# Performance work log

Hardware: AMD Instinct MI355X
Metric: run time of the kernel (lower is better)

The kernel has to match this reference:

```python
import jax, jax.numpy as jnp
import numpy as np


def _mha(q, k, v, num_heads):
    # q,k,v: [B, L, C] -> multi-head attention, scale = 1/sqrt(head_dim)
    B, Lq, C = q.shape
    Lk = k.shape[1]
    d = C // num_heads
    qh = q.reshape(B, Lq, num_heads, d)
    kh = k.reshape(B, Lk, num_heads, d)
    vh = v.reshape(B, Lk, num_heads, d)
    scale = 1.0 / jnp.sqrt(jnp.asarray(d, q.dtype))
    scores = jnp.einsum('blhd,bmhd->bhlm', qh, kh) * scale
    probs = jax.nn.softmax(scores, axis=-1)
    out = jnp.einsum('bhlm,bmhd->blhd', probs, vh)
    return out.reshape(B, Lq, C)


def setup_inputs() -> dict:
    key = jax.random.key(0)
    ks = jax.random.split(key, 9)
    b, n, f, l, C = 1, 4, 8, 256, 320
    s = 0.02
    return {
        'hidden_states': jax.random.normal(ks[0], (b * n * f, l, C), jnp.float32),
        'Wq': jax.random.normal(ks[1], (C, C), jnp.float32) * s,
        'Wk': jax.random.normal(ks[2], (C, C), jnp.float32) * s,
        'Wv': jax.random.normal(ks[3], (C, C), jnp.float32) * s,
        'Wo': jax.random.normal(ks[4], (C, C), jnp.float32) * s,
        'bo': jnp.zeros((C,), jnp.float32),
        'Wq_i2v': jax.random.normal(ks[5], (C, C), jnp.float32) * s,
        'Wo_i2v': jax.random.normal(ks[6], (C, C), jnp.float32) * s,
        'bo_i2v': jnp.zeros((C,), jnp.float32),
        'num_heads': 8,
        'num_views': 4,
        'num_frames': 8,
    }


def reference(hidden_states, Wq, Wk, Wv, Wo, bo, Wq_i2v, Wo_i2v, bo_i2v,
              num_heads, num_views, num_frames):
    BNF, l, C = hidden_states.shape
    n, f = num_views, num_frames
    b = BNF // (n * f)
    # '(b n f) l c -> (b f) (n l) c'
    h = hidden_states.reshape(b, n, f, l, C).transpose(0, 2, 1, 3, 4).reshape(b * f, n * l, C)
    L = n * l

    q = h @ Wq
    k = h @ Wk
    v = h @ Wv

    # first-frame KV broadcast across all frames within the same b
    k_first = jnp.broadcast_to(k.reshape(b, f, L, C)[:, 0:1], (b, f, L, C)).reshape(b * f, L, C)
    v_first = jnp.broadcast_to(v.reshape(b, f, L, C)[:, 0:1], (b, f, L, C)).reshape(b * f, L, C)

    base = _mha(q, k, v, num_heads)

    q_i2v = h @ Wq_i2v
    i2v = _mha(q_i2v, k_first, v_first, num_heads)
    i2v = i2v @ Wo_i2v + bo_i2v

    out = (base + i2v) @ Wo + bo

    # '(b f) (n l) c -> (b n f) l c'
    out = out.reshape(b, f, n, l, C).transpose(0, 2, 1, 3, 4).reshape(b * n * f, l, C)
    return out
```

## Files before the change

kernel.cpp:

```cpp
#include <hip/hip_runtime.h>

#define MROWS 8192
#define CDIM  320
#define QPAD  512

typedef __attribute__((ext_vector_type(8))) short bf16x8;
typedef __attribute__((ext_vector_type(4))) float f32x4;

__device__ __forceinline__ unsigned bfbits(float x) {
  union { float f; unsigned u; } a; a.f = x;
  return a.u + 0x8000u;
}
__device__ __forceinline__ unsigned pack2bf(float a, float b) {
  return (bfbits(a) >> 16) | (bfbits(b) & 0xffff0000u);
}
__device__ __forceinline__ void splitbf(float x, short& hi, short& lo) {
  unsigned hu = bfbits(x) & 0xffff0000u;
  union { unsigned u; float f; } h; h.u = hu;
  hi = (short)(hu >> 16);
  lo = (short)(bfbits(x - h.f) >> 16);
}

__device__ __forceinline__ int swizzle_row(int r) {
  int ff = r >> 10;
  int t  = r & 1023;
  int nn = t >> 8;
  int ll = t & 255;
  return nn * 2048 + ff * 256 + ll;
}

__global__ __launch_bounds__(256) void wc_kernel(
    const float* __restrict__ Woi, const float* __restrict__ Wo,
    float* __restrict__ Wc)
{
  const int r0 = blockIdx.x * 64, c0 = blockIdx.y * 64;
  __shared__ float As[64][36];
  __shared__ float Bs[32][68];
  const int tid = threadIdx.x, tx = tid & 15, ty = tid >> 4;
  float acc[4][4] = {};

  const int ra = tid >> 3, kq = (tid & 7) * 4;
  const int kb = tid >> 4, cq = (tid & 15) * 4;

  for (int k0 = 0; k0 < 320; k0 += 32) {
    float4 a1 = *(const float4*)(Woi + (size_t)(r0 + ra) * 320 + k0 + kq);
    float4 a2 = *(const float4*)(Woi + (size_t)(r0 + ra + 32) * 320 + k0 + kq);
    float4 b1 = *(const float4*)(Wo + (size_t)(k0 + kb) * 320 + c0 + cq);
    float4 b2 = *(const float4*)(Wo + (size_t)(k0 + kb + 16) * 320 + c0 + cq);
    __syncthreads();
    *(float4*)&As[ra][kq] = a1;
    *(float4*)&As[ra + 32][kq] = a2;
    *(float4*)&Bs[kb][cq] = b1;
    *(float4*)&Bs[kb + 16][cq] = b2;
    __syncthreads();
    #pragma unroll
    for (int kk = 0; kk < 32; ++kk) {
      float4 bv = *(const float4*)&Bs[kk][tx * 4];
      #pragma unroll
      for (int i = 0; i < 4; ++i) {
        float a = As[ty * 4 + i][kk];
        acc[i][0] = fmaf(a, bv.x, acc[i][0]);
        acc[i][1] = fmaf(a, bv.y, acc[i][1]);
        acc[i][2] = fmaf(a, bv.z, acc[i][2]);
        acc[i][3] = fmaf(a, bv.w, acc[i][3]);
      }
    }
  }
  #pragma unroll
  for (int i = 0; i < 4; ++i) {
    float4 v = make_float4(acc[i][0], acc[i][1], acc[i][2], acc[i][3]);
    *(float4*)(Wc + (size_t)(r0 + ty * 4 + i) * 320 + c0 + tx * 4) = v;
  }
}

__global__ __launch_bounds__(256) void pack_kernel(
    const float* __restrict__ hidden,
    const float* __restrict__ Wq, const float* __restrict__ Wk,
    const float* __restrict__ Wv, const float* __restrict__ Wqi,
    const float* __restrict__ Wo, const float* __restrict__ Wc,
    const float* __restrict__ bo, const float* __restrict__ boi,
    short* __restrict__ Ah, short* __restrict__ Al,
    short* __restrict__ WTh, short* __restrict__ WTl,
    short* __restrict__ WFh, short* __restrict__ WFl,
    float* __restrict__ bc,
    short* __restrict__ Qp, short* __restrict__ Kp, short* __restrict__ Qip,
    float qscale)
{
  const int b = blockIdx.x, tid = threadIdx.x;
  if (b < 64) {
    const int r0 = b * 128;
    for (int e = tid; e < 128 * 80; e += 256) {
      int r = e / 80, cq = (e % 80) * 4;
      float4 x = *(const float4*)(hidden + (size_t)swizzle_row(r0 + r) * 320 + cq);
      union { ushort4 v; short s[4]; } h, l;
      splitbf(x.x, h.s[0], l.s[0]); splitbf(x.y, h.s[1], l.s[1]);
      splitbf(x.z, h.s[2], l.s[2]); splitbf(x.w, h.s[3], l.s[3]);
      *(ushort4*)&Ah[(size_t)(r0 + r) * 320 + cq] = h.v;
      *(ushort4*)&Al[(size_t)(r0 + r) * 320 + cq] = l.v;
    }
  } else if (b < 128) {
    const int t2 = b - 64, wi = t2 >> 4, seg = t2 & 15;
    const float* W = wi == 0 ? Wq : wi == 1 ? Wk : wi == 2 ? Wv : Wqi;
    const float s = (wi == 0 || wi == 3) ? qscale : 1.0f;
    short* th = WTh + (size_t)wi * 320 * 320;
    short* tl = WTl + (size_t)wi * 320 * 320;
    for (int e = tid; e < 20 * 320; e += 256) {
      int n = seg * 20 + e / 320, k = e % 320;
      short hi, lo;
      splitbf(W[(size_t)k * 320 + n] * s, hi, lo);
      th[(size_t)n * 320 + k] = hi;
      tl[(size_t)n * 320 + k] = lo;
    }
  } else if (b < 160) {
    const int t2 = b - 128;
    for (int e = tid; e < 10 * 640; e += 256) {
      int n = t2 * 10 + e / 640, k = e % 640;
      float x = (k < 320) ? Wo[(size_t)k * 320 + n] : Wc[(size_t)(k - 320) * 320 + n];
      short hi, lo;
      splitbf(x, hi, lo);
      WFh[(size_t)n * 640 + k] = hi;
      WFl[(size_t)n * 640 + k] = lo;
    }
  } else if (b < 168) {
    const int n = (b - 160) * 40 + tid;
    if (tid < 40) {
      float s = bo[n];
      for (int j = 0; j < 320; ++j) s = fmaf(boi[j], Wo[(size_t)j * 320 + n], s);
      bc[n] = s;
    }
  } else {
    const int bz = b - 168, buf = bz >> 5, seg = bz & 31;
    short* P = buf == 0 ? Qp : buf == 1 ? Kp : Qip;
    const uint4 z = make_uint4(0, 0, 0, 0);
    for (int e = tid; e < 256 * 24; e += 256) {
      int row = (seg << 8) + (e / 24);
      int cc = e % 24, h = cc / 3, c3 = cc % 3;
      *(uint4*)&P[(size_t)row * QPAD + h * 64 + 40 + c3 * 8] = z;
    }
  }
}

__global__ __launch_bounds__(256, 3) void mfma_gemm(
    const short* __restrict__ Ah, const short* __restrict__ Al,
    const short* __restrict__ BTh, const short* __restrict__ BTl,
    int K, int mode,
    short* __restrict__ Qp, short* __restrict__ Kp,
    short* __restrict__ Vt, short* __restrict__ Qip,
    float* __restrict__ Of, const float* __restrict__ bias)
{
  const int tid  = threadIdx.x;
  const int wave = tid >> 6;
  const int lane = tid & 63;
  const int quad = lane >> 4;
  const int l16  = lane & 15;
  const int row0 = blockIdx.x * 128;

  const short *bth, *btl;
  int nbase, wi = 0;
  if (mode == 0) {
    const int ct = blockIdx.y;
    wi = ct / 5;
    bth = BTh + (size_t)wi * 320 * 320;
    btl = BTl + (size_t)wi * 320 * 320;
    nbase = (ct % 5) * 64;
  } else {
    bth = BTh; btl = BTl;
    nbase = blockIdx.y * 64;
  }

  __shared__ short Ash[128][40], Asl[128][40];
  __shared__ short Bsh[64][40],  Bsl[64][40];

  f32x4 acc[2][4];
  #pragma unroll
  for (int mt = 0; mt < 2; ++mt)
    #pragma unroll
    for (int nt = 0; nt < 4; ++nt) acc[mt][nt] = (f32x4){0.f, 0.f, 0.f, 0.f};

  const int ar = tid >> 2, akc = (tid & 3) * 8;
  const int bn = tid >> 2, bkc = (tid & 3) * 8;

  const short* pa_h = Ah + (size_t)(row0 + ar) * K + akc;
  const short* pa_l = Al ? Al + (size_t)(row0 + ar) * K + akc : nullptr;
  const short* pb_h = bth + (size_t)(nbase + bn) * K + bkc;
  const short* pb_l = btl + (size_t)(nbase + bn) * K + bkc;

  for (int k0 = 0; k0 < K; k0 += 32) {
    uint4 ah1 = *(const uint4*)(pa_h + k0);
    uint4 ah2 = *(const uint4*)(pa_h + (size_t)64 * K + k0);
    uint4 al1, al2;
    if (Al) {
      al1 = *(const uint4*)(pa_l + k0);
      al2 = *(const uint4*)(pa_l + (size_t)64 * K + k0);
    }
    uint4 bh = *(const uint4*)(pb_h + k0);
    uint4 bl = *(const uint4*)(pb_l + k0);
    __syncthreads();
    *(uint4*)&Ash[ar][akc]      = ah1;
    *(uint4*)&Ash[ar + 64][akc] = ah2;
    if (Al) {
      *(uint4*)&Asl[ar][akc]      = al1;
      *(uint4*)&Asl[ar + 64][akc] = al2;
    }
    *(uint4*)&Bsh[bn][bkc] = bh;
    *(uint4*)&Bsl[bn][bkc] = bl;
    __syncthreads();

    bf16x8 afh[2], afl[2], bfh[4], bfl[4];
    #pragma unroll
    for (int mt = 0; mt < 2; ++mt) {
      afh[mt] = *(const bf16x8*)&Ash[wave * 32 + mt * 16 + l16][quad * 8];
      if (Al) afl[mt] = *(const bf16x8*)&Asl[wave * 32 + mt * 16 + l16][quad * 8];
    }
    #pragma unroll
    for (int nt = 0; nt < 4; ++nt) {
      bfh[nt] = *(const bf16x8*)&Bsh[nt * 16 + l16][quad * 8];
      bfl[nt] = *(const bf16x8*)&Bsl[nt * 16 + l16][quad * 8];
    }
    #pragma unroll
    for (int mt = 0; mt < 2; ++mt)
      #pragma unroll
      for (int nt = 0; nt < 4; ++nt) {
        acc[mt][nt] = __builtin_amdgcn_mfma_f32_16x16x32_bf16(afh[mt], bfh[nt], acc[mt][nt], 0, 0, 0);
        acc[mt][nt] = __builtin_amdgcn_mfma_f32_16x16x32_bf16(afh[mt], bfl[nt], acc[mt][nt], 0, 0, 0);
        if (Al)
          acc[mt][nt] = __builtin_amdgcn_mfma_f32_16x16x32_bf16(afl[mt], bfh[nt], acc[mt][nt], 0, 0, 0);
      }
  }

  if (mode == 0) {
    if (wi == 2) {
      #pragma unroll
      for (int mt = 0; mt < 2; ++mt)
        #pragma unroll
        for (int nt = 0; nt < 4; ++nt) {
          const int col  = nbase + nt * 16 + l16;
          const int rowb = row0 + wave * 32 + mt * 16 + quad * 4;
          union { ushort4 v; short s[4]; } pk;
          #pragma unroll
          for (int r = 0; r < 4; ++r) pk.s[r] = (short)(bfbits(acc[mt][nt][r]) >> 16);
          *(ushort4*)&Vt[(size_t)col * MROWS + rowb] = pk.v;
        }
    } else {
      short* Op = wi == 0 ? Qp : wi == 1 ? Kp : Qip;
      #pragma unroll
      for (int mt = 0; mt < 2; ++mt)
        #pragma unroll
        for (int nt = 0; nt < 4; ++nt) {
          const int col  = nbase + nt * 16 + l16;
          const int h    = col / 40;
          const int pcol = h * 64 + (col - h * 40);
          const int rowb = row0 + wave * 32 + mt * 16 + quad * 4;
          #pragma unroll
          for (int r = 0; r < 4; ++r)
            Op[(size_t)(rowb + r) * QPAD + pcol] = (short)(bfbits(acc[mt][nt][r]) >> 16);
        }
    }
  } else {
    #pragma unroll
    for (int mt = 0; mt < 2; ++mt)
      #pragma unroll
      for (int nt = 0; nt < 4; ++nt) {
        const int col  = nbase + nt * 16 + l16;
        const int rowb = row0 + wave * 32 + mt * 16 + quad * 4;
        const float bb = bias[col];
        #pragma unroll
        for (int r = 0; r < 4; ++r)
          Of[(size_t)swizzle_row(rowb + r) * CDIM + col] = acc[mt][nt][r] + bb;
      }
  }
}

__global__ __launch_bounds__(256, 4) void attn_kernel(
    const short* __restrict__ Qp, const short* __restrict__ Qip,
    const short* __restrict__ Kp, const short* __restrict__ Vtg,
    short* __restrict__ AOh)
{
  const int qblk = blockIdx.x;
  const int hh   = blockIdx.y;
  const int zz   = blockIdx.z;
  const int var  = zz >> 3;
  const int bf   = zz & 7;
  const int tid  = threadIdx.x;
  const int wave = tid >> 6;
  const int lane = tid & 63;
  const int quad = lane >> 4;
  const int l16  = lane & 15;

  const short* Q = var ? Qip : Qp;
  const int kvbase = var ? 0 : (bf << 10);
  const int coff = var * 320 + hh * 40;

  __shared__ short Ks[64][80];
  __shared__ short Vt[48][72];
  __shared__ short Ps[4][2][16][72];

  if (tid < 64) {
    *(uint4*)&Vt[40 + (tid >> 3)][(tid & 7) * 8] = make_uint4(0, 0, 0, 0);
  }

  bf16x8 qf0[2], qf1[2];
  #pragma unroll
  for (int qt = 0; qt < 2; ++qt) {
    const short* qp = Q + (size_t)((bf << 10) + (qblk << 7) + (wave << 5) + (qt << 4) + l16) * QPAD + hh * 64;
    qf0[qt] = *(const bf16x8*)(qp + quad * 8);
    qf1[qt] = *(const bf16x8*)(qp + 32 + quad * 8);
  }

  f32x4 acc[2][3];
  float lsum[2] = {0.f, 0.f};
  #pragma unroll
  for (int qt = 0; qt < 2; ++qt)
    #pragma unroll
    for (int t = 0; t < 3; ++t) acc[qt][t] = (f32x4){0.f, 0.f, 0.f, 0.f};

  const short* Kb = Kp + (size_t)kvbase * QPAD + hh * 64;
  const short* Vb = Vtg + (size_t)(hh * 40) * MROWS + kvbase;

  const int gbase = (l16 & 3) + ((l16 >> 2) << 4);

  for (int s0 = 0; s0 < 1024; s0 += 64) {
    __syncthreads();
    #pragma unroll
    for (int pass = 0; pass < 4; ++pass) {
      int u = tid + (pass << 8);
      if (u < 512) {
        int key = u >> 3, c = u & 7;
        *(uint4*)&Ks[key][c * 8] =
            *(const uint4*)(Kb + (size_t)(s0 + key) * QPAD + c * 8);
      } else if (u < 832) {
        int v = u - 512;
        int dcol = v >> 3, ch = v & 7;
        *(uint4*)&Vt[dcol][ch * 8] =
            *(const uint4*)(Vb + (size_t)dcol * MROWS + s0 + ch * 8);
      }
    }
    __syncthreads();

    bf16x8 kb0[4], kb1[4];
    #pragma unroll
    for (int kt = 0; kt < 4; ++kt) {
      const short* kr = &Ks[gbase + 4 * kt][quad * 8];
      kb0[kt] = *(const bf16x8*)kr;
      kb1[kt] = *(const bf16x8*)(kr + 32);
    }

    #pragma unroll
    for (int qt = 0; qt < 2; ++qt) {
      unsigned pbuf[8];
      float ls = 0.f;
      #pragma unroll
      for (int kt = 0; kt < 4; ++kt) {
        f32x4 st = (f32x4){0.f, 0.f, 0.f, 0.f};
        st = __builtin_amdgcn_mfma_f32_16x16x32_bf16(kb0[kt], qf0[qt], st, 0, 0, 0);
        st = __builtin_amdgcn_mfma_f32_16x16x32_bf16(kb1[kt], qf1[qt], st, 0, 0, 0);
        float p0 = __expf(st[0]);
        float p1 = __expf(st[1]);
        float p2 = __expf(st[2]);
        float p3 = __expf(st[3]);
        ls += (p0 + p1) + (p2 + p3);
        pbuf[kt * 2]     = pack2bf(p0, p1);
        pbuf[kt * 2 + 1] = pack2bf(p2, p3);
      }
      lsum[qt] += ls;

      *(uint4*)&Ps[wave][qt][l16][quad * 16]     = *(uint4*)&pbuf[0];
      *(uint4*)&Ps[wave][qt][l16][quad * 16 + 8] = *(uint4*)&pbuf[4];

      asm volatile("s_waitcnt lgkmcnt(0)" ::: "memory");

      bf16x8 pa0 = *(const bf16x8*)&Ps[wave][qt][l16][quad * 8];
      bf16x8 pa1 = *(const bf16x8*)&Ps[wave][qt][l16][32 + quad * 8];
      #pragma unroll
      for (int t = 0; t < 3; ++t) {
        bf16x8 v0 = *(const bf16x8*)&Vt[t * 16 + l16][quad * 8];
        bf16x8 v1 = *(const bf16x8*)&Vt[t * 16 + l16][32 + quad * 8];
        acc[qt][t] = __builtin_amdgcn_mfma_f32_16x16x32_bf16(pa0, v0, acc[qt][t], 0, 0, 0);
        acc[qt][t] = __builtin_amdgcn_mfma_f32_16x16x32_bf16(pa1, v1, acc[qt][t], 0, 0, 0);
      }
    }
  }

  #pragma unroll
  for (int qt = 0; qt < 2; ++qt) {
    float li = lsum[qt];
    li += __shfl_xor(li, 16);
    li += __shfl_xor(li, 32);
    float inv = 1.f / li;
    float invr[4];
    #pragma unroll
    for (int r = 0; r < 4; ++r) invr[r] = __shfl(inv, quad * 4 + r, 64);

    const int baserow = (bf << 10) + (qblk << 7) + (wave << 5) + (qt << 4) + quad * 4;
    #pragma unroll
    for (int t = 0; t < 3; ++t) {
      int dcol = t * 16 + l16;
      if (dcol < 40) {
        short* op = AOh + (size_t)baserow * 640 + coff + dcol;
        #pragma unroll
        for (int r = 0; r < 4; ++r)
          op[(size_t)r * 640] = (short)(bfbits(acc[qt][t][r] * invr[r]) >> 16);
      }
    }
  }
}

extern "C" void kernel_launch(void* const* d_in, const int* in_sizes, int n_in,
                              void* d_out, int out_size, void* d_ws, size_t ws_size,
                              hipStream_t stream) {
  const float* hidden  = (const float*)d_in[0];
  const float* Wq      = (const float*)d_in[1];
  const float* Wk      = (const float*)d_in[2];
  const float* Wv      = (const float*)d_in[3];
  const float* Wo      = (const float*)d_in[4];
  const float* bo      = (const float*)d_in[5];
  const float* Wq_i2v  = (const float*)d_in[6];
  const float* Wo_i2v  = (const float*)d_in[7];
  const float* bo_i2v  = (const float*)d_in[8];
  float* out = (float*)d_out;

  const size_t SZ  = (size_t)MROWS * CDIM;
  const size_t SZP = (size_t)MROWS * QPAD;
  short* Ah  = (short*)d_ws;
  short* Al  = Ah + SZ;
  short* AOh = Ah;
  short* Qp  = Al + SZ;
  short* Kp  = Qp + SZP;
  short* Qip = Kp + SZP;
  short* Vt  = Qip + SZP;
  short* WTh = Vt + (size_t)328 * MROWS;
  short* WTl = WTh + 409600;
  short* WFh = WTl + 409600;
  short* WFl = WFh + 204800;
  float* Wc  = (float*)(WFl + 204800);
  float* bc  = Wc + 102400;

  const float qscale = 0.15811388300841898f;

  wc_kernel<<<dim3(5, 5), 256, 0, stream>>>(Wo_i2v, Wo, Wc);

  pack_kernel<<<dim3(264), 256, 0, stream>>>(
      hidden, Wq, Wk, Wv, Wq_i2v, Wo, Wc, bo, bo_i2v,
      Ah, Al, WTh, WTl, WFh, WFl, bc, Qp, Kp, Qip, qscale);

  mfma_gemm<<<dim3(64, 20), 256, 0, stream>>>(
      Ah, Al, WTh, WTl, 320, 0, Qp, Kp, Vt, Qip, nullptr, nullptr);

  attn_kernel<<<dim3(8, 8, 16), 256, 0, stream>>>(Qp, Qip, Kp, Vt, AOh);

  mfma_gemm<<<dim3(64, 5), 256, 0, stream>>>(
      AOh, nullptr, WFh, WFl, 640, 1, nullptr, nullptr, nullptr, nullptr, out, bc);
}
```

Baseline: 219.8 us.

## Register-prefetch next K/V tile and load only the live 40 head dims

The attention loop now issues the global loads for the next 64-key K and V tile into registers before computing on the current tile, so memory latency overlaps with the MFMA and exp work. K loads now copy only the 40 live head-dim columns (5 chunks per row) instead of 64, and the padded columns are zeroed once up front. The K row mapping and P-store layout are also rearranged so each K tile is loaded once and P is written per key tile. This costs extra registers for the prefetch buffers and adds uneven per-thread load assignment. The prefetch on the last iteration reads one tile past the end of the range.

Measured after the change: 227.2 us. 1.03x slower.

```diff
diff --git a/kernel.cpp b/kernel.cpp
--- a/kernel.cpp
+++ b/kernel.cpp
@@ -291,13 +291,13 @@
   const int kvbase = var ? 0 : (bf << 10);
   const int coff = var * 320 + hh * 40;
 
-  __shared__ short Ks[64][80];
+  __shared__ short Ks[64][72];
   __shared__ short Vt[48][72];
   __shared__ short Ps[4][2][16][72];
 
-  if (tid < 64) {
+  *(uint4*)&Ks[tid >> 2][40 + (tid & 3) * 8] = make_uint4(0, 0, 0, 0);
+  if (tid < 64)
     *(uint4*)&Vt[40 + (tid >> 3)][(tid & 7) * 8] = make_uint4(0, 0, 0, 0);
-  }
 
   bf16x8 qf0[2], qf1[2];
   #pragma unroll
@@ -317,66 +317,85 @@
   const short* Kb = Kp + (size_t)kvbase * QPAD + hh * 64;
   const short* Vb = Vtg + (size_t)(hh * 40) * MROWS + kvbase;
 
-  const int gbase = (l16 & 3) + ((l16 >> 2) << 4);
-
-  for (int s0 = 0; s0 < 1024; s0 += 64) {
-    __syncthreads();
-    #pragma unroll
-    for (int pass = 0; pass < 4; ++pass) {
-      int u = tid + (pass << 8);
-      if (u < 512) {
-        int key = u >> 3, c = u & 7;
-        *(uint4*)&Ks[key][c * 8] =
-            *(const uint4*)(Kb + (size_t)(s0 + key) * QPAD + c * 8);
-      } else if (u < 832) {
-        int v = u - 512;
-        int dcol = v >> 3, ch = v & 7;
-        *(uint4*)&Vt[dcol][ch * 8] =
-            *(const uint4*)(Vb + (size_t)dcol * MROWS + s0 + ch * 8);
-      }
-    }
-    __syncthreads();
-
-    bf16x8 kb0[4], kb1[4];
+  const int k1 = tid / 5, c1 = tid % 5;
+  const short* g1 = Kb + (size_t)k1 * QPAD + c1 * 8;
+  short*       s1 = &Ks[k1][c1 * 8];
+  const short* g2; short* s2; int inc2;
+  if (tid < 64) {
+    int u = tid + 256, k2 = u / 5, c2 = u % 5;
+    g2 = Kb + (size_t)k2 * QPAD + c2 * 8;
+    s2 = &Ks[k2][c2 * 8];
+    inc2 = 64 * QPAD;
+  } else {
+    int v = tid - 64;
+    g2 = Vb + (size_t)(v >> 3) * MROWS + (v & 7) * 8;
+    s2 = &Vt[v >> 3][(v & 7) * 8];
+    inc2 = 64;
+  }
+  const short* g3 = nullptr; short* s3 = nullptr;
+  if (tid < 128) {
+    int v = tid + 192;
+    g3 = Vb + (size_t)(v >> 3) * MROWS + (v & 7) * 8;
+    s3 = &Vt[v >> 3][(v & 7) * 8];
+  }
+
+  uint4 r1 = *(const uint4*)g1;
+  uint4 r2 = *(const uint4*)g2;
+  uint4 r3 = make_uint4(0, 0, 0, 0);
+  if (tid < 128) r3 = *(const uint4*)g3;
+
+  for (int step = 0; step < 16; ++step) {
+    __syncthreads();
+    *(uint4*)s1 = r1;
+    *(uint4*)s2 = r2;
+    if (tid < 128) *(uint4*)s3 = r3;
+    __syncthreads();
+
+    g1 += (size_t)64 * QPAD;
+    g2 += inc2;
+    r1 = *(const uint4*)g1;
+    r2 = *(const uint4*)g2;
+    if (tid < 128) { g3 += 64; r3 = *(const uint4*)g3; }
+
+    bf16x8 vf[2][3];
+    #pragma unroll
+    for (int kh = 0; kh < 2; ++kh)
+      #pragma unroll
+      for (int t = 0; t < 3; ++t)
+        vf[kh][t] = *(const bf16x8*)&Vt[t * 16 + l16][kh * 32 + quad * 8];
+
     #pragma unroll
     for (int kt = 0; kt < 4; ++kt) {
-      const short* kr = &Ks[gbase + 4 * kt][quad * 8];
-      kb0[kt] = *(const bf16x8*)kr;
-      kb1[kt] = *(const bf16x8*)(kr + 32);
-    }
-
-    #pragma unroll
-    for (int qt = 0; qt < 2; ++qt) {
-      unsigned pbuf[8];
-      float ls = 0.f;
-      #pragma unroll
-      for (int kt = 0; kt < 4; ++kt) {
+      const short* kr = &Ks[kt * 16 + l16][quad * 8];
+      bf16x8 kb0 = *(const bf16x8*)kr;
+      bf16x8 kb1 = *(const bf16x8*)(kr + 32);
+      #pragma unroll
+      for (int qt = 0; qt < 2; ++qt) {
         f32x4 st = (f32x4){0.f, 0.f, 0.f, 0.f};
-        st = __builtin_amdgcn_mfma_f32_16x16x32_bf16(kb0[kt], qf0[qt], st, 0, 0, 0);
-        st = __builtin_amdgcn_mfma_f32_16x16x32_bf16(kb1[kt], qf1[qt], st, 0, 0, 0);
+        st = __builtin_amdgcn_mfma_f32_16x16x32_bf16(kb0, qf0[qt], st, 0, 0, 0);
+        st = __builtin_amdgcn_mfma_f32_16x16x32_bf16(kb1, qf1[qt], st, 0, 0, 0);
         float p0 = __expf(st[0]);
         float p1 = __expf(st[1]);
         float p2 = __expf(st[2]);
         float p3 = __expf(st[3]);
-        ls += (p0 + p1) + (p2 + p3);
-        pbuf[kt * 2]     = pack2bf(p0, p1);
-        pbuf[kt * 2 + 1] = pack2bf(p2, p3);
-      }
-      lsum[qt] += ls;
-
-      *(uint4*)&Ps[wave][qt][l16][quad * 16]     = *(uint4*)&pbuf[0];
-      *(uint4*)&Ps[wave][qt][l16][quad * 16 + 8] = *(uint4*)&pbuf[4];
-
-      asm volatile("s_waitcnt lgkmcnt(0)" ::: "memory");
-
+        lsum[qt] += (p0 + p1) + (p2 + p3);
+        uint2 pk;
+        pk.x = pack2bf(p0, p1);
+        pk.y = pack2bf(p2, p3);
+        *(uint2*)&Ps[wave][qt][l16][kt * 16 + quad * 4] = pk;
+      }
+    }
+
+    asm volatile("s_waitcnt lgkmcnt(0)" ::: "memory");
+
+    #pragma unroll
+    for (int qt = 0; qt < 2; ++qt) {
       bf16x8 pa0 = *(const bf16x8*)&Ps[wave][qt][l16][quad * 8];
       bf16x8 pa1 = *(const bf16x8*)&Ps[wave][qt][l16][32 + quad * 8];
       #pragma unroll
       for (int t = 0; t < 3; ++t) {
-        bf16x8 v0 = *(const bf16x8*)&Vt[t * 16 + l16][quad * 8];
-        bf16x8 v1 = *(const bf16x8*)&Vt[t * 16 + l16][32 + quad * 8];
-        acc[qt][t] = __builtin_amdgcn_mfma_f32_16x16x32_bf16(pa0, v0, acc[qt][t], 0, 0, 0);
-        acc[qt][t] = __builtin_amdgcn_mfma_f32_16x16x32_bf16(pa1, v1, acc[qt][t], 0, 0, 0);
+        acc[qt][t] = __builtin_amdgcn_mfma_f32_16x16x32_bf16(pa0, vf[0][t], acc[qt][t], 0, 0, 0);
+        acc[qt][t] = __builtin_amdgcn_mfma_f32_16x16x32_bf16(pa1, vf[1][t], acc[qt][t], 0, 0, 0);
       }
     }
   }
```
